# Optimization experiments

Measured on AMD Instinct MI355X. Metric: run time of the kernel, lower is better.

Reference implementation:

```python
import jax, jax.numpy as jnp
import numpy as np

B, S, HID = 1, 2048, 2048
H, HKV, D = 16, 4, 128
GROUPS = H // HKV
SCALE = D ** -0.5


def rotate_half(x):
    x1, x2 = x[..., : x.shape[-1] // 2], x[..., x.shape[-1] // 2 :]
    return jnp.concatenate((-x2, x1), axis=-1)


def setup_inputs() -> dict:
    key = jax.random.key(0)
    ks = jax.random.split(key, 8)
    hidden_states = jax.random.normal(ks[0], (B, S, HID), dtype=jnp.float32)
    # standard RoPE tables, base 10000
    inv_freq = 1.0 / (10000.0 ** (np.arange(0, D, 2, dtype=np.float32) / D))
    t = np.arange(S, dtype=np.float32)
    freqs = np.outer(t, inv_freq)                      # (S, D/2)
    emb = np.concatenate([freqs, freqs], axis=-1)      # (S, D)
    cos = jnp.asarray(np.cos(emb)[None], dtype=jnp.float32)  # (1, S, D)
    sin = jnp.asarray(np.sin(emb)[None], dtype=jnp.float32)
    std = 0.02
    Wq = jax.random.normal(ks[1], (HID, H * D), dtype=jnp.float32) * std
    Wk = jax.random.normal(ks[2], (HID, HKV * D), dtype=jnp.float32) * std
    Wv = jax.random.normal(ks[3], (HID, HKV * D), dtype=jnp.float32) * std
    Wg = jax.random.normal(ks[4], (HID, HKV), dtype=jnp.float32) * std
    Wo = jax.random.normal(ks[5], (H * D, HID), dtype=jnp.float32) * std
    return {"hidden_states": hidden_states, "cos": cos, "sin": sin,
            "Wq": Wq, "Wk": Wk, "Wv": Wv, "Wg": Wg, "Wo": Wo}


def reference(hidden_states, cos, sin, Wq, Wk, Wv, Wg, Wo):
    b, s, _ = hidden_states.shape
    # projections -> (B, heads, S, D)
    q = (hidden_states @ Wq).reshape(b, s, H, D).transpose(0, 2, 1, 3)
    k = (hidden_states @ Wk).reshape(b, s, HKV, D).transpose(0, 2, 1, 3)
    v = (hidden_states @ Wv).reshape(b, s, HKV, D).transpose(0, 2, 1, 3)
    g = (hidden_states @ Wg).transpose(0, 2, 1)                 # (B, HKV, S)
    g = jax.nn.log_sigmoid(g.astype(jnp.float32))
    # RoPE
    c, sn = cos[:, None, :, :], sin[:, None, :, :]
    q = q * c + rotate_half(q) * sn
    k = k * c + rotate_half(k) * sn
    # GQA repeat kv heads
    k = jnp.repeat(k, GROUPS, axis=1)
    v = jnp.repeat(v, GROUPS, axis=1)
    g = jnp.repeat(g, GROUPS, axis=1)                           # (B, H, S)
    # gated power retention, deg=2, parallel (quadratic) form
    G = jnp.cumsum(g, axis=-1)                                  # (B, H, S)
    # decay_ij = exp(G_i - G_j) for j <= i  (<= 1 since logsigmoid < 0)
    logdecay = G[..., :, None] - G[..., None, :]                # (B, H, S, S)
    causal = jnp.tril(jnp.ones((s, s), dtype=bool))
    decay = jnp.where(causal, jnp.exp(logdecay), 0.0)
    qk = jnp.einsum("bhid,bhjd->bhij", q, k) * SCALE
    scores = (qk * qk) * decay                                  # deg=2 power scores
    den = jnp.maximum(jnp.sum(scores, axis=-1, keepdims=True), 1.0)
    out = jnp.einsum("bhij,bhjd->bhid", scores, v) / den        # (B, H, S, D)
    out = out.transpose(0, 2, 1, 3).reshape(b, s, H * D)
    return out @ Wo
```

## Files before the change

### kernel.cpp

```cpp
#include <hip/hip_runtime.h>
#include <hip/hip_bf16.h>

#define S_LEN 2048
#define HID   2048
#define NH    16
#define NKV   4
#define HD    128
#define KVD   512
#define NQKV  3072
#define SCALE2 0.0078125f
#define NCH   80

typedef __bf16 bf16;
typedef __attribute__((ext_vector_type(8))) __bf16 bf16x8;
typedef __attribute__((ext_vector_type(4))) float f32x4;

__device__ __forceinline__ void gload_lds16(const bf16* g, bf16* l) {
    __builtin_amdgcn_global_load_lds((const __attribute__((address_space(1))) void*)g,
                                     (__attribute__((address_space(3))) void*)l, 16, 0, 0);
}

__device__ __forceinline__ void transpose_tile(const float* __restrict__ W,
                                               bf16* __restrict__ Wt,
                                               int K, int N, int bx, int by,
                                               int t, float (*Ts)[65])
{
    const int kb = bx * 64, nb = by * 64;
    const int tr = t >> 6, tc = t & 63;
    #pragma unroll
    for (int p = 0; p < 16; ++p) {
        int k = p * 4 + tr;
        Ts[k][tc] = W[(size_t)(kb + k) * N + nb + tc];
    }
    __syncthreads();
    const int nr = t >> 3, kc = t & 7;
    #pragma unroll
    for (int p = 0; p < 2; ++p) {
        int n = p * 32 + nr;
        bf16x8 o;
        #pragma unroll
        for (int x = 0; x < 8; ++x) o[x] = (bf16)Ts[kc * 8 + x][n];
        *(bf16x8*)&Wt[(size_t)(nb + n) * K + kb + kc * 8] = o;
    }
}

__global__ __launch_bounds__(256) void prep_kernel(const float* __restrict__ hs,
                                                   const float* __restrict__ Wq,
                                                   const float* __restrict__ Wk,
                                                   const float* __restrict__ Wv,
                                                   const float* __restrict__ Wo,
                                                   const float* __restrict__ Wg,
                                                   bf16* __restrict__ hsb,
                                                   bf16* __restrict__ WcatT,
                                                   bf16* __restrict__ WoT,
                                                   float* __restrict__ graw,
                                                   float* __restrict__ outz)
{
    __shared__ float Ts[64][65];
    const int b = blockIdx.x, tid = threadIdx.x;

    if (b < 2048) {
        int i = (b * 256 + tid) * 8;
        const float4* qp = (const float4*)&hs[i];
        float4 a = qp[0], c = qp[1];
        bf16x8 r;
        r[0]=(bf16)a.x; r[1]=(bf16)a.y; r[2]=(bf16)a.z; r[3]=(bf16)a.w;
        r[4]=(bf16)c.x; r[5]=(bf16)c.y; r[6]=(bf16)c.z; r[7]=(bf16)c.w;
        *(bf16x8*)&hsb[i] = r;
    } else if (b < 3072) {
        int lb = b - 2048;
        transpose_tile(Wq, WcatT, HID, HID, lb >> 5, lb & 31, tid, Ts);
    } else if (b < 3328) {
        int lb = b - 3072;
        transpose_tile(Wk, WcatT + (size_t)2048 * HID, HID, KVD, lb >> 3, lb & 7, tid, Ts);
    } else if (b < 3584) {
        int lb = b - 3328;
        transpose_tile(Wv, WcatT + (size_t)2560 * HID, HID, KVD, lb >> 3, lb & 7, tid, Ts);
    } else if (b < 4608) {
        int lb = b - 3584;
        transpose_tile(Wo, WoT, HID, HID, lb >> 5, lb & 31, tid, Ts);
    } else if (b < 6656) {
        int i = ((b - 4608) * 256 + tid) * 8;
        float4 z = make_float4(0.f, 0.f, 0.f, 0.f);
        *(float4*)&outz[i] = z;
        *(float4*)&outz[i + 4] = z;
    } else {
        const int w = tid >> 6, lane = tid & 63;
        const int s = (b - 6656) * 4 + w;
        float a0 = 0.f, a1 = 0.f, a2 = 0.f, a3 = 0.f;
        for (int kk = lane; kk < HID; kk += 64) {
            float h = hs[(size_t)s * HID + kk];
            const float* wr = &Wg[kk * 4];
            a0 += h * wr[0]; a1 += h * wr[1];
            a2 += h * wr[2]; a3 += h * wr[3];
        }
        #pragma unroll
        for (int off = 32; off >= 1; off >>= 1) {
            a0 += __shfl_xor(a0, off); a1 += __shfl_xor(a1, off);
            a2 += __shfl_xor(a2, off); a3 += __shfl_xor(a3, off);
        }
        if (lane == 0) {
            float vv[4] = {a0, a1, a2, a3};
            #pragma unroll
            for (int c = 0; c < 4; ++c) {
                float x = vv[c];
                graw[c * S_LEN + s] = fminf(x, 0.f) - log1pf(expf(-fabsf(x)));
            }
        }
    }
}

__device__ __forceinline__ void gemm128_pipe(const bf16* __restrict__ A,
                                             const bf16* __restrict__ Bt,
                                             int K, int k0, int nt, int mb, int nb,
                                             bf16 (*As)[128][32], bf16 (*Bs)[128][32],
                                             f32x4 (*acc)[4],
                                             int w, int l16, int quad, int lane)
{
    const int m0 = (w & 1) * 64, n0 = (w >> 1) * 64;
    const int srow = lane >> 2, scol = (lane & 3) * 8;
    const bf16* a0 = &A [(size_t)(mb + w * 32 +      srow) * K + k0 + scol];
    const bf16* a1 = &A [(size_t)(mb + w * 32 + 16 + srow) * K + k0 + scol];
    const bf16* b0 = &Bt[(size_t)(nb + w * 32 +      srow) * K + k0 + scol];
    const bf16* b1 = &Bt[(size_t)(nb + w * 32 + 16 + srow) * K + k0 + scol];

#define ISSUE_TILE(T, BUF) do {                                         \
        gload_lds16(a0 + (size_t)(T) * 32, &As[BUF][w * 32     ][0]);   \
        gload_lds16(a1 + (size_t)(T) * 32, &As[BUF][w * 32 + 16][0]);   \
        gload_lds16(b0 + (size_t)(T) * 32, &Bs[BUF][w * 32     ][0]);   \
        gload_lds16(b1 + (size_t)(T) * 32, &Bs[BUF][w * 32 + 16][0]);   \
    } while (0)

    ISSUE_TILE(0, 0);
    ISSUE_TILE(1, 1);
    asm volatile("s_waitcnt vmcnt(4)" ::: "memory");
    __builtin_amdgcn_s_barrier();
    __builtin_amdgcn_sched_barrier(0);

    int cb = 0;
    for (int t = 0; t < nt; ++t) {
        bf16x8 af[4], bfr[4];
        #pragma unroll
        for (int x = 0; x < 4; ++x) af[x]  = *(const bf16x8*)&As[cb][m0 + x * 16 + l16][quad * 8];
        #pragma unroll
        for (int u = 0; u < 4; ++u) bfr[u] = *(const bf16x8*)&Bs[cb][n0 + u * 16 + l16][quad * 8];
        #pragma unroll
        for (int x = 0; x < 4; ++x)
            #pragma unroll
            for (int u = 0; u < 4; ++u)
                acc[x][u] = __builtin_amdgcn_mfma_f32_16x16x32_bf16(af[x], bfr[u], acc[x][u], 0, 0, 0);

        if (t + 2 < nt) {
            const int ib = (cb == 0) ? 2 : cb - 1;
            ISSUE_TILE(t + 2, ib);
            asm volatile("s_waitcnt vmcnt(4)" ::: "memory");
            __builtin_amdgcn_s_barrier();
            __builtin_amdgcn_sched_barrier(0);
        } else if (t + 1 < nt) {
            asm volatile("s_waitcnt vmcnt(0)" ::: "memory");
            __builtin_amdgcn_s_barrier();
            __builtin_amdgcn_sched_barrier(0);
        }
        cb = (cb == 2) ? 0 : cb + 1;
    }
#undef ISSUE_TILE
}

__global__ __launch_bounds__(256) void gemm_qkv_kernel(const bf16* __restrict__ A,
                                                       const bf16* __restrict__ Wt,
                                                       float* __restrict__ qsl,
                                                       float* __restrict__ ksl,
                                                       float* __restrict__ vsl,
                                                       int M, int K)
{
    __shared__ __attribute__((aligned(16))) bf16 As[3][128][32];
    __shared__ __attribute__((aligned(16))) bf16 Bs[3][128][32];
    const int tid = threadIdx.x, w = tid >> 6, lane = tid & 63;
    const int l16 = lane & 15, quad = lane >> 4;
    const int mb = blockIdx.x * 128, nb = blockIdx.y * 128;
    const int m0 = (w & 1) * 64, n0 = (w >> 1) * 64;
    const int z = blockIdx.z, kh = K >> 1, k0 = z * kh;

    float* qd = qsl + (size_t)z * S_LEN * HID;
    float* kd = ksl + (size_t)z * S_LEN * KVD;
    float* vd = vsl + (size_t)z * S_LEN * KVD;

    f32x4 acc[4][4] = {};
    gemm128_pipe(A, Wt, K, k0, kh >> 5, mb, nb, As, Bs, acc, w, l16, quad, lane);

    #pragma unroll
    for (int t = 0; t < 4; ++t)
        #pragma unroll
        for (int u = 0; u < 4; ++u)
            #pragma unroll
            for (int r = 0; r < 4; ++r) {
                int row = mb + m0 + t * 16 + quad * 4 + r;
                int col = nb + n0 + u * 16 + l16;
                float val = acc[t][u][r];
                if (nb < 2048)       qd[(size_t)row * HID + col] = val;
                else if (nb < 2560)  kd[(size_t)row * KVD + (col - 2048)] = val;
                else                 vd[(size_t)(col - 2560) * S_LEN + row] = val;
            }
}

__global__ __launch_bounds__(256) void gemm_wo_kernel(const bf16* __restrict__ A,
                                                      const bf16* __restrict__ Bt,
                                                      float* __restrict__ C,
                                                      int M, int N, int K)
{
    __shared__ __attribute__((aligned(16))) bf16 As[3][128][32];
    __shared__ __attribute__((aligned(16))) bf16 Bs[3][128][32];
    const int tid = threadIdx.x, w = tid >> 6, lane = tid & 63;
    const int l16 = lane & 15, quad = lane >> 4;
    const int mb = blockIdx.x * 128, nb = blockIdx.y * 128;
    const int m0 = (w & 1) * 64, n0 = (w >> 1) * 64;
    const int kh = K >> 1, k0 = blockIdx.z * kh;

    f32x4 acc[4][4] = {};
    gemm128_pipe(A, Bt, K, k0, kh >> 5, mb, nb, As, Bs, acc, w, l16, quad, lane);

    #pragma unroll
    for (int t = 0; t < 4; ++t)
        #pragma unroll
        for (int u = 0; u < 4; ++u)
            #pragma unroll
            for (int r = 0; r < 4; ++r) {
                int row = mb + m0 + t * 16 + quad * 4 + r;
                int col = nb + n0 + u * 16 + l16;
                unsafeAtomicAdd(&C[(size_t)row * N + col], acc[t][u][r]);
            }
}

#define RQB (S_LEN * NH * 64 / 256)
#define RKB (S_LEN * NKV * 64 / 256)
#define RVB (S_LEN * KVD / 8 / 256)
__global__ __launch_bounds__(256) void rope_kernel(const float* __restrict__ qsl,
                                                   const float* __restrict__ ksl,
                                                   const float* __restrict__ vsl,
                                                   bf16* __restrict__ qb,
                                                   bf16* __restrict__ kb,
                                                   bf16* __restrict__ vT,
                                                   const float* __restrict__ cosb,
                                                   const float* __restrict__ sinb,
                                                   const float* __restrict__ graw,
                                                   float* __restrict__ G)
{
    const int blk = blockIdx.x;
    if (blk < RQB + RKB) {
        int idx = blk * 256 + threadIdx.x;
        const float* src; size_t ssz; bf16* dst; int s, rem, stride;
        if (blk < RQB) {
            src = qsl; ssz = (size_t)S_LEN * HID; dst = qb; stride = HID;
            s = idx / (NH * 64); rem = idx % (NH * 64);
        } else {
            idx -= RQB * 256;
            src = ksl; ssz = (size_t)S_LEN * KVD; dst = kb; stride = KVD;
            s = idx / (NKV * 64); rem = idx % (NKV * 64);
        }
        int h = rem >> 6, d = rem & 63;
        size_t base = (size_t)s * stride + h * 128 + d;
        float x0 = src[base]      + src[ssz + base];
        float x1 = src[base + 64] + src[ssz + base + 64];
        float c0 = cosb[s * 128 + d], c1 = cosb[s * 128 + d + 64];
        float n0 = sinb[s * 128 + d], n1 = sinb[s * 128 + d + 64];
        dst[base]      = (bf16)(x0 * c0 - x1 * n0);
        dst[base + 64] = (bf16)(x1 * c1 + x0 * n1);
    } else if (blk < RQB + RKB + RVB) {
        int i = ((blk - RQB - RKB) * 256 + threadIdx.x) * 8;
        const size_t ssz = (size_t)S_LEN * KVD;
        bf16x8 r;
        #pragma unroll
        for (int x = 0; x < 8; ++x) r[x] = (bf16)(vsl[i + x] + vsl[ssz + i + x]);
        *(bf16x8*)&vT[i] = r;
    } else {
        const int c = blk - (RQB + RKB + RVB);
        const int t = threadIdx.x;
        __shared__ float sums[256];
        float loc[8];
        float run = 0.f;
        #pragma unroll
        for (int i = 0; i < 8; ++i) { run += graw[c * S_LEN + t * 8 + i]; loc[i] = run; }
        sums[t] = run;
        __syncthreads();
        for (int off = 1; off < 256; off <<= 1) {
            float add = (t >= off) ? sums[t - off] : 0.f;
            __syncthreads();
            sums[t] += add;
            __syncthreads();
        }
        float offset = sums[t] - run;
        #pragma unroll
        for (int i = 0; i < 8; ++i) G[c * S_LEN + t * 8 + i] = offset + loc[i];
    }
}

__global__ __launch_bounds__(256) void attn_kernel(const bf16* __restrict__ q,
                                                   const bf16* __restrict__ k,
                                                   const bf16* __restrict__ vT,
                                                   const float* __restrict__ G,
                                                   bf16* __restrict__ out,
                                                   float* __restrict__ pO,
                                                   float* __restrict__ pden)
{
    int rem = blockIdx.x, qt = 0, cch = 0;
    #pragma unroll
    for (int g = 0; g < 4; ++g) {
        int sz = 8 * (g + 1);
        if (rem < sz) { qt = g * 8 + rem / (g + 1); cch = rem % (g + 1); break; }
        rem -= sz;
    }
    const int gg = qt >> 3, nc = gg + 1;
    const int jt0 = cch * 8, jt1 = min(qt + 1, jt0 + 8);

    const int h = blockIdx.y, kvh = h >> 2;
    const int qb = qt * 64;
    const int tid = threadIdx.x, w = tid >> 6, lane = tid & 63;
    const int l16 = lane & 15, quad = lane >> 4;

    __shared__ __attribute__((aligned(16))) bf16 Ks4[4][64][32];
    __shared__ __attribute__((aligned(16))) bf16 Vt4[2][128][32];
    __shared__ __attribute__((aligned(16))) bf16 Sb[4][16][68];

    bf16x8 qf[4];
    const int qrow = qb + w * 16 + l16;
    #pragma unroll
    for (int kc = 0; kc < 4; ++kc)
        qf[kc] = *(const bf16x8*)&q[(size_t)qrow * HID + h * HD + kc * 32 + quad * 8];

    const int irow = qb + w * 16 + quad * 4;
    float Gq[4];
    #pragma unroll
    for (int r = 0; r < 4; ++r) Gq[r] = G[kvh * S_LEN + irow + r];

    const int sr4 = lane >> 2, sc4 = (lane & 3) * 8;
    const int vkk = w >> 1, vdg = (w & 1) * 4;

    f32x4 acco[8] = {};
    float den[4] = {0.f, 0.f, 0.f, 0.f};

    for (int kt = jt0; kt < jt1; ++kt) {
        const int jb = kt * 64;
        __syncthreads();
        #pragma unroll
        for (int rg = 0; rg < 4; ++rg)
            gload_lds16(&k[(size_t)(jb + rg * 16 + sr4) * KVD + kvh * HD + w * 32 + sc4],
                        &Ks4[w][rg * 16][0]);
        #pragma unroll
        for (int it = 0; it < 4; ++it)
            gload_lds16(&vT[(size_t)(kvh * HD + (vdg + it) * 16 + sr4) * S_LEN + jb + vkk * 32 + sc4],
                        &Vt4[vkk][(vdg + it) * 16][0]);
        __syncthreads();

        f32x4 accs[4] = {};
        #pragma unroll
        for (int t = 0; t < 4; ++t)
            #pragma unroll
            for (int kc = 0; kc < 4; ++kc) {
                bf16x8 bfr = *(const bf16x8*)&Ks4[kc][t * 16 + l16][quad * 8];
                accs[t] = __builtin_amdgcn_mfma_f32_16x16x32_bf16(qf[kc], bfr, accs[t], 0, 0, 0);
            }

        const float Gt = G[kvh * S_LEN + jb];
        float sr[4];
        #pragma unroll
        for (int r = 0; r < 4; ++r) sr[r] = SCALE2 * __expf(Gq[r] - Gt);
        #pragma unroll
        for (int t = 0; t < 4; ++t) {
            int j = jb + t * 16 + l16;
            float colF = __expf(fminf(Gt - G[kvh * S_LEN + j], 85.f));
            #pragma unroll
            for (int r = 0; r < 4; ++r) {
                float d0 = accs[t][r];
                float sc = (j <= irow + r) ? d0 * d0 * sr[r] * colF : 0.f;
                den[r] += sc;
                Sb[w][quad * 4 + r][t * 16 + l16] = (bf16)sc;
            }
        }

        #pragma unroll
        for (int kk = 0; kk < 2; ++kk) {
            bf16x8 af = *(const bf16x8*)&Sb[w][l16][kk * 32 + quad * 8];
            #pragma unroll
            for (int dt = 0; dt < 8; ++dt) {
                bf16x8 bfr = *(const bf16x8*)&Vt4[kk][dt * 16 + l16][quad * 8];
                acco[dt] = __builtin_amdgcn_mfma_f32_16x16x32_bf16(af, bfr, acco[dt], 0, 0, 0);
            }
        }
    }

    #pragma unroll
    for (int r = 0; r < 4; ++r) {
        #pragma unroll
        for (int off = 1; off < 16; off <<= 1) den[r] += __shfl_xor(den[r], off);
    }

    if (nc == 1) {
        float dinv[4];
        #pragma unroll
        for (int r = 0; r < 4; ++r) dinv[r] = 1.f / fmaxf(den[r], 1.f);
        #pragma unroll
        for (int dt = 0; dt < 8; ++dt)
            #pragma unroll
            for (int r = 0; r < 4; ++r)
                out[(size_t)(irow + r) * HID + h * HD + dt * 16 + l16] =
                    (bf16)(acco[dt][r] * dinv[r]);
    } else {
        const int slot = h * NCH + 4 * gg * (gg + 1) + (qt & 7) * (gg + 1) + cch;
        float* po = &pO[(size_t)slot * 8192];
        const int lr = w * 16 + quad * 4;
        #pragma unroll
        for (int dt = 0; dt < 8; ++dt)
            #pragma unroll
            for (int r = 0; r < 4; ++r)
                po[(lr + r) * 128 + dt * 16 + l16] = acco[dt][r];
        if (l16 == 0) {
            #pragma unroll
            for (int r = 0; r < 4; ++r) pden[slot * 64 + lr + r] = den[r];
        }
    }
}

__global__ __launch_bounds__(256) void attn_reduce_kernel(const float* __restrict__ pO,
                                                          const float* __restrict__ pden,
                                                          bf16* __restrict__ out)
{
    const int p = blockIdx.x;
    const int h = p / 24, qt = 8 + p % 24;
    const int gg = qt >> 3, nc = gg + 1;
    const int base = h * NCH + 4 * gg * (gg + 1) + (qt & 7) * (gg + 1);
    const int qb = qt * 64;
    const int tid = threadIdx.x;

    __shared__ float sden[64];
    if (tid < 64) {
        float s = 0.f;
        for (int c = 0; c < nc; ++c) s += pden[(base + c) * 64 + tid];
        sden[tid] = 1.f / fmaxf(s, 1.f);
    }
    __syncthreads();

    #pragma unroll
    for (int i = 0; i < 8; ++i) {
        int e = i * 1024 + tid * 4;
        float4 s = make_float4(0.f, 0.f, 0.f, 0.f);
        for (int c = 0; c < nc; ++c) {
            float4 v = *(const float4*)&pO[(size_t)(base + c) * 8192 + e];
            s.x += v.x; s.y += v.y; s.z += v.z; s.w += v.w;
        }
        int lr = e >> 7, col = e & 127;
        float di = sden[lr];
        bf16* o = &out[(size_t)(qb + lr) * HID + h * HD + col];
        o[0] = (bf16)(s.x * di); o[1] = (bf16)(s.y * di);
        o[2] = (bf16)(s.z * di); o[3] = (bf16)(s.w * di);
    }
}

extern "C" void kernel_launch(void* const* d_in, const int* in_sizes, int n_in,
                              void* d_out, int out_size, void* d_ws, size_t ws_size,
                              hipStream_t stream)
{
    const float* hs   = (const float*)d_in[0];
    const float* cosb = (const float*)d_in[1];
    const float* sinb = (const float*)d_in[2];
    const float* Wq   = (const float*)d_in[3];
    const float* Wk   = (const float*)d_in[4];
    const float* Wv   = (const float*)d_in[5];
    const float* Wg   = (const float*)d_in[6];
    const float* Wo   = (const float*)d_in[7];
    float* out = (float*)d_out;

    char* p = (char*)d_ws;
    bf16*  qbuf  = (bf16*)p;  p += (size_t)S_LEN * HID * 2;
    bf16*  kbuf  = (bf16*)p;  p += (size_t)S_LEN * KVD * 2;
    bf16*  vT    = (bf16*)p;  p += (size_t)S_LEN * KVD * 2;
    bf16*  abuf  = (bf16*)p;  p += (size_t)S_LEN * HID * 2;
    bf16*  hsb   = (bf16*)p;  p += (size_t)S_LEN * HID * 2;
    bf16*  WcatT = (bf16*)p;  p += (size_t)NQKV * HID * 2;
    bf16*  WoT   = (bf16*)p;  p += (size_t)HID * HID * 2;
    float* graw  = (float*)p; p += (size_t)NKV * S_LEN * 4;
    float* G     = (float*)p; p += (size_t)NKV * S_LEN * 4;
    float* pO    = (float*)p; p += (size_t)NH * NCH * 8192 * 4;
    float* pden  = (float*)p; p += (size_t)NH * NCH * 64 * 4;

    float* qsl = pO;
    float* ksl = pO + (size_t)8 * 1024 * 1024;
    float* vsl = (float*)abuf;

    prep_kernel<<<7168, 256, 0, stream>>>(hs, Wq, Wk, Wv, Wo, Wg,
                                          hsb, WcatT, WoT, graw, out);
    gemm_qkv_kernel<<<dim3(16, 24, 2), 256, 0, stream>>>(hsb, WcatT, qsl, ksl, vsl, S_LEN, HID);
    rope_kernel<<<RQB + RKB + RVB + NKV, 256, 0, stream>>>(qsl, ksl, vsl, qbuf, kbuf, vT,
                                                           cosb, sinb, graw, G);
    attn_kernel<<<dim3(NCH, NH), 256, 0, stream>>>(qbuf, kbuf, vT, G, abuf, pO, pden);
    attn_reduce_kernel<<<NH * 24, 256, 0, stream>>>(pO, pden, abuf);
    gemm_wo_kernel<<<dim3(16, 16, 2), 256, 0, stream>>>(abuf, WoT, out, S_LEN, HID, HID);
}
```

Baseline: 299.5 us.

## Split-K by four with atomic accumulation and double-buffered GEMM pipeline

Raises the K split of both projection GEMMs from two to four and has the QKV GEMM accumulate into zeroed fp32 buffers with atomics instead of writing separate partial slices that rope later sums. The prep kernel gains extra blocks to zero the QKV accumulators. The GEMM inner loop drops from triple to double buffering with a simpler wait/barrier pattern. The aim is more blocks for occupancy and less partial-sum traffic in rope, at the cost of atomic contention, extra zeroing, and less load/compute overlap.

```diff
diff --git a/kernel.cpp b/kernel.cpp
--- a/kernel.cpp
+++ b/kernel.cpp
@@ -54,7 +54,8 @@
                                                    bf16* __restrict__ WcatT,
                                                    bf16* __restrict__ WoT,
                                                    float* __restrict__ graw,
-                                                   float* __restrict__ outz)
+                                                   float* __restrict__ outz,
+                                                   float* __restrict__ qkvz)
 {
     __shared__ float Ts[64][65];
     const int b = blockIdx.x, tid = threadIdx.x;
@@ -84,7 +85,7 @@
         float4 z = make_float4(0.f, 0.f, 0.f, 0.f);
         *(float4*)&outz[i] = z;
         *(float4*)&outz[i + 4] = z;
-    } else {
+    } else if (b < 7168) {
         const int w = tid >> 6, lane = tid & 63;
         const int s = (b - 6656) * 4 + w;
         float a0 = 0.f, a1 = 0.f, a2 = 0.f, a3 = 0.f;
@@ -107,15 +108,20 @@
                 graw[c * S_LEN + s] = fminf(x, 0.f) - log1pf(expf(-fabsf(x)));
             }
         }
-    }
-}
-
-__device__ __forceinline__ void gemm128_pipe(const bf16* __restrict__ A,
-                                             const bf16* __restrict__ Bt,
-                                             int K, int k0, int nt, int mb, int nb,
-                                             bf16 (*As)[128][32], bf16 (*Bs)[128][32],
-                                             f32x4 (*acc)[4],
-                                             int w, int l16, int quad, int lane)
+    } else {
+        int i = ((b - 7168) * 256 + tid) * 8;
+        float4 z = make_float4(0.f, 0.f, 0.f, 0.f);
+        *(float4*)&qkvz[i] = z;
+        *(float4*)&qkvz[i + 4] = z;
+    }
+}
+
+__device__ __forceinline__ void gemm128_db(const bf16* __restrict__ A,
+                                           const bf16* __restrict__ Bt,
+                                           int K, int k0, int nt, int mb, int nb,
+                                           bf16 (*As)[128][32], bf16 (*Bs)[128][32],
+                                           f32x4 (*acc)[4],
+                                           int w, int l16, int quad, int lane)
 {
     const int m0 = (w & 1) * 64, n0 = (w >> 1) * 64;
     const int srow = lane >> 2, scol = (lane & 3) * 8;
@@ -132,13 +138,18 @@
     } while (0)
 
     ISSUE_TILE(0, 0);
-    ISSUE_TILE(1, 1);
-    asm volatile("s_waitcnt vmcnt(4)" ::: "memory");
-    __builtin_amdgcn_s_barrier();
-    __builtin_amdgcn_sched_barrier(0);
-
-    int cb = 0;
+
     for (int t = 0; t < nt; ++t) {
+        const int cb = t & 1;
+        if (t + 1 < nt) {
+            ISSUE_TILE(t + 1, cb ^ 1);
+            asm volatile("s_waitcnt vmcnt(4)" ::: "memory");
+        } else {
+            asm volatile("s_waitcnt vmcnt(0)" ::: "memory");
+        }
+        __builtin_amdgcn_s_barrier();
+        __builtin_amdgcn_sched_barrier(0);
+
         bf16x8 af[4], bfr[4];
         #pragma unroll
         for (int x = 0; x < 4; ++x) af[x]  = *(const bf16x8*)&As[cb][m0 + x * 16 + l16][quad * 8];
@@ -150,43 +161,30 @@
             for (int u = 0; u < 4; ++u)
                 acc[x][u] = __builtin_amdgcn_mfma_f32_16x16x32_bf16(af[x], bfr[u], acc[x][u], 0, 0, 0);
 
-        if (t + 2 < nt) {
-            const int ib = (cb == 0) ? 2 : cb - 1;
-            ISSUE_TILE(t + 2, ib);
-            asm volatile("s_waitcnt vmcnt(4)" ::: "memory");
+        __builtin_amdgcn_sched_barrier(0);
+        if (t + 1 < nt)
             __builtin_amdgcn_s_barrier();
-            __builtin_amdgcn_sched_barrier(0);
-        } else if (t + 1 < nt) {
-            asm volatile("s_waitcnt vmcnt(0)" ::: "memory");
-            __builtin_amdgcn_s_barrier();
-            __builtin_amdgcn_sched_barrier(0);
-        }
-        cb = (cb == 2) ? 0 : cb + 1;
     }
 #undef ISSUE_TILE
 }
 
 __global__ __launch_bounds__(256) void gemm_qkv_kernel(const bf16* __restrict__ A,
                                                        const bf16* __restrict__ Wt,
-                                                       float* __restrict__ qsl,
-                                                       float* __restrict__ ksl,
-                                                       float* __restrict__ vsl,
+                                                       float* __restrict__ qacc,
+                                                       float* __restrict__ kacc,
+                                                       float* __restrict__ vacc,
                                                        int M, int K)
 {
-    __shared__ __attribute__((aligned(16))) bf16 As[3][128][32];
-    __shared__ __attribute__((aligned(16))) bf16 Bs[3][128][32];
+    __shared__ __attribute__((aligned(16))) bf16 As[2][128][32];
+    __shared__ __attribute__((aligned(16))) bf16 Bs[2][128][32];
     const int tid = threadIdx.x, w = tid >> 6, lane = tid & 63;
     const int l16 = lane & 15, quad = lane >> 4;
     const int mb = blockIdx.x * 128, nb = blockIdx.y * 128;
     const int m0 = (w & 1) * 64, n0 = (w >> 1) * 64;
-    const int z = blockIdx.z, kh = K >> 1, k0 = z * kh;
-
-    float* qd = qsl + (size_t)z * S_LEN * HID;
-    float* kd = ksl + (size_t)z * S_LEN * KVD;
-    float* vd = vsl + (size_t)z * S_LEN * KVD;
+    const int z = blockIdx.z, kh = K >> 2, k0 = z * kh;
 
     f32x4 acc[4][4] = {};
-    gemm128_pipe(A, Wt, K, k0, kh >> 5, mb, nb, As, Bs, acc, w, l16, quad, lane);
+    gemm128_db(A, Wt, K, k0, kh >> 5, mb, nb, As, Bs, acc, w, l16, quad, lane);
 
     #pragma unroll
     for (int t = 0; t < 4; ++t)
@@ -197,9 +195,9 @@
                 int row = mb + m0 + t * 16 + quad * 4 + r;
                 int col = nb + n0 + u * 16 + l16;
                 float val = acc[t][u][r];
-                if (nb < 2048)       qd[(size_t)row * HID + col] = val;
-                else if (nb < 2560)  kd[(size_t)row * KVD + (col - 2048)] = val;
-                else                 vd[(size_t)(col - 2560) * S_LEN + row] = val;
+                if (nb < 2048)       unsafeAtomicAdd(&qacc[(size_t)row * HID + col], val);
+                else if (nb < 2560)  unsafeAtomicAdd(&kacc[(size_t)row * KVD + (col - 2048)], val);
+                else                 unsafeAtomicAdd(&vacc[(size_t)(col - 2560) * S_LEN + row], val);
             }
 }
 
@@ -208,16 +206,16 @@
                                                       float* __restrict__ C,
                                                       int M, int N, int K)
 {
-    __shared__ __attribute__((aligned(16))) bf16 As[3][128][32];
-    __shared__ __attribute__((aligned(16))) bf16 Bs[3][128][32];
+    __shared__ __attribute__((aligned(16))) bf16 As[2][128][32];
+    __shared__ __attribute__((aligned(16))) bf16 Bs[2][128][32];
     const int tid = threadIdx.x, w = tid >> 6, lane = tid & 63;
     const int l16 = lane & 15, quad = lane >> 4;
     const int mb = blockIdx.x * 128, nb = blockIdx.y * 128;
     const int m0 = (w & 1) * 64, n0 = (w >> 1) * 64;
-    const int kh = K >> 1, k0 = blockIdx.z * kh;
+    const int kh = K >> 2, k0 = blockIdx.z * kh;
 
     f32x4 acc[4][4] = {};
-    gemm128_pipe(A, Bt, K, k0, kh >> 5, mb, nb, As, Bs, acc, w, l16, quad, lane);
+    gemm128_db(A, Bt, K, k0, kh >> 5, mb, nb, As, Bs, acc, w, l16, quad, lane);
 
     #pragma unroll
     for (int t = 0; t < 4; ++t)
@@ -234,9 +232,9 @@
 #define RQB (S_LEN * NH * 64 / 256)
 #define RKB (S_LEN * NKV * 64 / 256)
 #define RVB (S_LEN * KVD / 8 / 256)
-__global__ __launch_bounds__(256) void rope_kernel(const float* __restrict__ qsl,
-                                                   const float* __restrict__ ksl,
-                                                   const float* __restrict__ vsl,
+__global__ __launch_bounds__(256) void rope_kernel(const float* __restrict__ qacc,
+                                                   const float* __restrict__ kacc,
+                                                   const float* __restrict__ vacc,
                                                    bf16* __restrict__ qb,
                                                    bf16* __restrict__ kb,
                                                    bf16* __restrict__ vT,
@@ -248,29 +246,28 @@
     const int blk = blockIdx.x;
     if (blk < RQB + RKB) {
         int idx = blk * 256 + threadIdx.x;
-        const float* src; size_t ssz; bf16* dst; int s, rem, stride;
+        const float* src; bf16* dst; int s, rem, stride;
         if (blk < RQB) {
-            src = qsl; ssz = (size_t)S_LEN * HID; dst = qb; stride = HID;
+            src = qacc; dst = qb; stride = HID;
             s = idx / (NH * 64); rem = idx % (NH * 64);
         } else {
             idx -= RQB * 256;
-            src = ksl; ssz = (size_t)S_LEN * KVD; dst = kb; stride = KVD;
+            src = kacc; dst = kb; stride = KVD;
             s = idx / (NKV * 64); rem = idx % (NKV * 64);
         }
         int h = rem >> 6, d = rem & 63;
         size_t base = (size_t)s * stride + h * 128 + d;
-        float x0 = src[base]      + src[ssz + base];
-        float x1 = src[base + 64] + src[ssz + base + 64];
+        float x0 = src[base];
+        float x1 = src[base + 64];
         float c0 = cosb[s * 128 + d], c1 = cosb[s * 128 + d + 64];
         float n0 = sinb[s * 128 + d], n1 = sinb[s * 128 + d + 64];
         dst[base]      = (bf16)(x0 * c0 - x1 * n0);
         dst[base + 64] = (bf16)(x1 * c1 + x0 * n1);
     } else if (blk < RQB + RKB + RVB) {
         int i = ((blk - RQB - RKB) * 256 + threadIdx.x) * 8;
-        const size_t ssz = (size_t)S_LEN * KVD;
         bf16x8 r;
         #pragma unroll
-        for (int x = 0; x < 8; ++x) r[x] = (bf16)(vsl[i + x] + vsl[ssz + i + x]);
+        for (int x = 0; x < 8; ++x) r[x] = (bf16)vacc[i + x];
         *(bf16x8*)&vT[i] = r;
     } else {
         const int c = blk - (RQB + RKB + RVB);
@@ -482,16 +479,16 @@
     float* pO    = (float*)p; p += (size_t)NH * NCH * 8192 * 4;
     float* pden  = (float*)p; p += (size_t)NH * NCH * 64 * 4;
 
-    float* qsl = pO;
-    float* ksl = pO + (size_t)8 * 1024 * 1024;
-    float* vsl = (float*)abuf;
-
-    prep_kernel<<<7168, 256, 0, stream>>>(hs, Wq, Wk, Wv, Wo, Wg,
-                                          hsb, WcatT, WoT, graw, out);
-    gemm_qkv_kernel<<<dim3(16, 24, 2), 256, 0, stream>>>(hsb, WcatT, qsl, ksl, vsl, S_LEN, HID);
-    rope_kernel<<<RQB + RKB + RVB + NKV, 256, 0, stream>>>(qsl, ksl, vsl, qbuf, kbuf, vT,
+    float* qacc = pO;
+    float* kacc = pO + (size_t)4 * 1024 * 1024;
+    float* vacc = pO + (size_t)5 * 1024 * 1024;
+
+    prep_kernel<<<10240, 256, 0, stream>>>(hs, Wq, Wk, Wv, Wo, Wg,
+                                           hsb, WcatT, WoT, graw, out, qacc);
+    gemm_qkv_kernel<<<dim3(16, 24, 4), 256, 0, stream>>>(hsb, WcatT, qacc, kacc, vacc, S_LEN, HID);
+    rope_kernel<<<RQB + RKB + RVB + NKV, 256, 0, stream>>>(qacc, kacc, vacc, qbuf, kbuf, vT,
                                                            cosb, sinb, graw, G);
     attn_kernel<<<dim3(NCH, NH), 256, 0, stream>>>(qbuf, kbuf, vT, G, abuf, pO, pden);
     attn_reduce_kernel<<<NH * 24, 256, 0, stream>>>(pO, pden, abuf);
-    gemm_wo_kernel<<<dim3(16, 16, 2), 256, 0, stream>>>(abuf, WoT, out, S_LEN, HID, HID);
-}
+    gemm_wo_kernel<<<dim3(16, 16, 4), 256, 0, stream>>>(abuf, WoT, out, S_LEN, HID, HID);
+}
```

Measured after the change: 402.7 us. 34.4% more time.
